# Kernel optimization log

Hardware: AMD Instinct MI355X
Metric: run time of the kernel (lower is better)

The kernel has to match this reference:

```python
import jax, jax.numpy as jnp
import numpy as np

D_MODEL = 1024
NUM_HEADS = 16
D_IN = 1024

def setup_inputs() -> dict:
    key = jax.random.key(0)
    ks = jax.random.split(key, 5)
    scale = 1.0 / np.sqrt(D_IN)
    return {
        "in_features": jax.random.normal(ks[0], (4, 2048, D_IN), dtype=jnp.float32),
        "q_weight": jax.random.normal(ks[1], (D_MODEL, D_IN), dtype=jnp.float32) * scale,
        "k_weight": jax.random.normal(ks[2], (D_MODEL, D_IN), dtype=jnp.float32) * scale,
        "v_weight": jax.random.normal(ks[3], (D_MODEL, D_IN), dtype=jnp.float32) * scale,
        "o_weight": jax.random.normal(ks[4], (D_MODEL, D_MODEL), dtype=jnp.float32) * scale,
    }

def reference(in_features, q_weight, k_weight, v_weight, o_weight):
    batch, seq_len, _ = in_features.shape
    d_head = D_MODEL // NUM_HEADS
    # QKV projections (Linear with no bias: x @ W^T)
    q = jnp.einsum('bsi,di->bsd', in_features, q_weight)
    k = jnp.einsum('bsi,di->bsd', in_features, k_weight)
    v = jnp.einsum('bsi,di->bsd', in_features, v_weight)
    # split heads -> [b, h, s, d_head]
    q = q.reshape(batch, seq_len, NUM_HEADS, d_head).transpose(0, 2, 1, 3)
    k = k.reshape(batch, seq_len, NUM_HEADS, d_head).transpose(0, 2, 1, 3)
    v = v.reshape(batch, seq_len, NUM_HEADS, d_head).transpose(0, 2, 1, 3)
    # scaled dot-product attention (scale by per-head dim, as in SelfAttention)
    scores = jnp.einsum('bhqd,bhkd->bhqk', q, k) / jnp.sqrt(jnp.float32(d_head))
    probs = jax.nn.softmax(scores, axis=-1)
    ctx = jnp.einsum('bhqk,bhkd->bhqd', probs, v)
    # merge heads -> [b, s, d_model]
    ctx = ctx.transpose(0, 2, 1, 3).reshape(batch, seq_len, D_MODEL)
    # output projection
    return jnp.einsum('bsd,md->bsm', ctx, o_weight)
```

## Files before the change

kernel.cpp:

```cpp
#include <hip/hip_runtime.h>

typedef _Float16 half8 __attribute__((ext_vector_type(8)));
typedef _Float16 half4v __attribute__((ext_vector_type(4)));
typedef float f32x4 __attribute__((ext_vector_type(4)));
typedef float f32x16 __attribute__((ext_vector_type(16)));

__device__ __forceinline__ void gload_lds16(const _Float16* g, _Float16* l) {
    __builtin_amdgcn_global_load_lds(
        (const __attribute__((address_space(1))) void*)g,
        (__attribute__((address_space(3))) void*)l,
        16, 0, 0);
}

__global__ void cvt_f32_f16(const float* __restrict__ src, _Float16* __restrict__ dst, int n4) {
    int i = blockIdx.x * blockDim.x + threadIdx.x;
    if (i >= n4) return;
    f32x4 v = ((const f32x4*)src)[i];
    half4v h;
    h[0] = (_Float16)v[0]; h[1] = (_Float16)v[1];
    h[2] = (_Float16)v[2]; h[3] = (_Float16)v[3];
    ((half4v*)dst)[i] = h;
}

template<int MODE>
__global__ void gemm_nt(const _Float16* __restrict__ A,
                        const _Float16* __restrict__ Wbase,
                        void* __restrict__ outbase)
{
    constexpr int K = 1024;
    __shared__ _Float16 As[2][128 * 32];
    __shared__ _Float16 Bs[2][128 * 32];

    const int tid  = threadIdx.x;
    const int lane = tid & 63;
    const int w    = tid >> 6;
    const int wr   = w >> 1, wc = w & 1;
    const int lr   = lane & 15, lg = lane >> 4;
    const int brow = blockIdx.x * 128;
    const int bcol = blockIdx.y * 128;

    const _Float16* Bw = Wbase + (MODE == 0 ? (size_t)blockIdx.z * (1024u * 1024u) : 0);

    const int srow = w * 16 + (lane >> 2);
    const int scol = (lane & 3) * 8;
    const _Float16* Ag = A  + (size_t)(brow + srow) * K + scol;
    const _Float16* Bg = Bw + (size_t)(bcol + srow) * K + scol;

    auto stage = [&](int buf, int kt) {
        const _Float16* a0 = Ag + kt * 32;
        const _Float16* b0 = Bg + kt * 32;
        gload_lds16(a0,           &As[buf][w * 512]);
        gload_lds16(a0 + 64 * K,  &As[buf][w * 512 + 2048]);
        gload_lds16(b0,           &Bs[buf][w * 512]);
        gload_lds16(b0 + 64 * K,  &Bs[buf][w * 512 + 2048]);
    };

    f32x4 acc[4][4] = {};
    stage(0, 0);
    __syncthreads();

    for (int kt = 0; kt < K / 32; ++kt) {
        const int cur = kt & 1;
        if (kt + 1 < K / 32) stage(cur ^ 1, kt + 1);
        half8 af[4], bf[4];
#pragma unroll
        for (int mi = 0; mi < 4; ++mi)
            af[mi] = *(const half8*)&As[cur][(wr * 64 + mi * 16 + lr) * 32 + lg * 8];
#pragma unroll
        for (int ni = 0; ni < 4; ++ni)
            bf[ni] = *(const half8*)&Bs[cur][(wc * 64 + ni * 16 + lr) * 32 + lg * 8];
#pragma unroll
        for (int mi = 0; mi < 4; ++mi)
#pragma unroll
            for (int ni = 0; ni < 4; ++ni)
                acc[mi][ni] = __builtin_amdgcn_mfma_f32_16x16x32_f16(af[mi], bf[ni], acc[mi][ni], 0, 0, 0);
        __syncthreads();
    }

    if (MODE == 0) {
        _Float16* outp = (_Float16*)outbase + (size_t)blockIdx.z * (8192u * 1024u);
        if (blockIdx.z == 2) {
            _Float16* Ts = &As[0][0];
#pragma unroll
            for (int p = 0; p < 2; ++p) {
                if (wc == p) {
#pragma unroll
                    for (int mi = 0; mi < 4; ++mi)
#pragma unroll
                        for (int ni = 0; ni < 4; ++ni) {
                            int drow = ni * 16 + lr;
                            int s0   = wr * 64 + mi * 16 + lg * 4;
                            half4v o;
#pragma unroll
                            for (int r = 0; r < 4; ++r) o[r] = (_Float16)acc[mi][ni][r];
                            int byteoff = drow * 256 + s0 * 2;
                            byteoff ^= (drow & 7) << 4;
                            *(half4v*)((char*)Ts + byteoff) = o;
                        }
                }
                __syncthreads();
                {
                    int row   = tid >> 2;
                    int cbase = (tid & 3) * 4;
                    int gd = bcol + p * 64 + row;
                    int h = gd >> 6, dd = gd & 63;
                    int b = brow >> 11, sseq = brow & 2047;
                    _Float16* gout = outp + (((size_t)b * 16 + h) * 64 + dd) * 2048 + sseq;
#pragma unroll
                    for (int j = 0; j < 4; ++j) {
                        int c  = cbase + j;
                        int lc = c ^ (row & 7);
                        half8 v = *(const half8*)&Ts[row * 128 + lc * 8];
                        *(half8*)&gout[c * 8] = v;
                    }
                }
                __syncthreads();
            }
        } else {
            const float scale = (blockIdx.z == 0) ? 0.18033688f : 1.0f;
#pragma unroll
            for (int mi = 0; mi < 4; ++mi)
#pragma unroll
                for (int ni = 0; ni < 4; ++ni)
#pragma unroll
                    for (int r = 0; r < 4; ++r) {
                        int row = brow + wr * 64 + mi * 16 + lg * 4 + r;
                        int col = bcol + wc * 64 + ni * 16 + lr;
                        int b = row >> 11, s = row & 2047;
                        int h = col >> 6,  d = col & 63;
                        outp[(((size_t)b * 16 + h) * 2048 + s) * 64 + d] =
                            (_Float16)(acc[mi][ni][r] * scale);
                    }
        }
    } else {
        float* outp = (float*)outbase;
#pragma unroll
        for (int mi = 0; mi < 4; ++mi)
#pragma unroll
            for (int ni = 0; ni < 4; ++ni)
#pragma unroll
                for (int r = 0; r < 4; ++r) {
                    int row = brow + wr * 64 + mi * 16 + lg * 4 + r;
                    int col = bcol + wc * 64 + ni * 16 + lr;
                    outp[(size_t)row * 1024 + col] = acc[mi][ni][r];
                }
    }
}

__global__ __launch_bounds__(256, 4)
void attn_kernel(const _Float16* __restrict__ Q,
                 const _Float16* __restrict__ Kx,
                 const _Float16* __restrict__ Vt,
                 _Float16* __restrict__ Ctx)
{
    __shared__ _Float16 Ks[2][64 * 72];
    __shared__ _Float16 Vs[2][64 * 72];

    const int tid = threadIdx.x, lane = tid & 63, w = tid >> 6;
    const int l31 = lane & 31, hi = lane >> 5;
    const int bh = blockIdx.y, qblk = blockIdx.x;

    const _Float16* Qp  = Q  + ((size_t)bh * 2048 + qblk * 128) * 64;
    const _Float16* Kp  = Kx + (size_t)bh * 2048 * 64;
    const _Float16* Vtp = Vt + (size_t)bh * 64 * 2048;

    half8 qf[4];
#pragma unroll
    for (int ks = 0; ks < 4; ++ks)
        qf[ks] = *(const half8*)(Qp + (size_t)(w * 32 + l31) * 64 + ks * 16 + hi * 8);

    const int srow = tid >> 3;
    const int scol = (tid & 7) * 8;
    const _Float16* Kg0 = Kp  + (size_t)srow * 64   + scol;
    const _Float16* Vg0 = Vtp + (size_t)srow * 2048 + scol;
    const int ldso = srow * 72 + scol;

    f32x16 cacc[2] = {};
    float m = -1e30f, l = 0.f;

    half8 kr0, kr1, vr0, vr1;
    kr0 = *(const half8*)(Kg0);
    kr1 = *(const half8*)(Kg0 + 32 * 64);
    vr0 = *(const half8*)(Vg0);
    vr1 = *(const half8*)(Vg0 + 32 * 2048);
    *(half8*)&Ks[0][ldso]           = kr0;
    *(half8*)&Ks[0][ldso + 32 * 72] = kr1;
    *(half8*)&Vs[0][ldso]           = vr0;
    *(half8*)&Vs[0][ldso + 32 * 72] = vr1;
    __syncthreads();

    for (int t = 0; t < 32; ++t) {
        const int cur = t & 1;
        if (t < 31) {
            kr0 = *(const half8*)(Kg0 + (size_t)(t + 1) * 4096);
            kr1 = *(const half8*)(Kg0 + (size_t)(t + 1) * 4096 + 32 * 64);
        }

        f32x16 sf[2];
        __builtin_amdgcn_s_setprio(1);
#pragma unroll
        for (int kt = 0; kt < 2; ++kt) {
            f32x16 z = {};
#pragma unroll
            for (int ks = 0; ks < 4; ++ks) {
                half8 kf = *(const half8*)&Ks[cur][(kt * 32 + l31) * 72 + ks * 16 + hi * 8];
                z = __builtin_amdgcn_mfma_f32_32x32x16_f16(kf, qf[ks], z, 0, 0, 0);
            }
            sf[kt] = z;
        }
        __builtin_amdgcn_s_setprio(0);

        if (t < 31) {
            *(half8*)&Ks[cur ^ 1][ldso]           = kr0;
            *(half8*)&Ks[cur ^ 1][ldso + 32 * 72] = kr1;
            vr0 = *(const half8*)(Vg0 + (t + 1) * 64);
            vr1 = *(const half8*)(Vg0 + (t + 1) * 64 + 32 * 2048);
        }

        float pmax = -1e30f;
#pragma unroll
        for (int kt = 0; kt < 2; ++kt)
#pragma unroll
            for (int r = 0; r < 16; ++r) pmax = fmaxf(pmax, sf[kt][r]);
        pmax = fmaxf(pmax, __shfl_xor(pmax, 32, 64));

        if (!__all(pmax <= m + 8.0f)) {
            float mn = fmaxf(m, pmax);
            float sc = __builtin_amdgcn_exp2f(m - mn);
            cacc[0] = cacc[0] * sc;
            cacc[1] = cacc[1] * sc;
            l *= sc;
            m = mn;
        }

        float rsum = 0.f;
#pragma unroll
        for (int kt = 0; kt < 2; ++kt)
#pragma unroll
            for (int r = 0; r < 16; ++r) {
                float p = __builtin_amdgcn_exp2f(sf[kt][r] - m);
                sf[kt][r] = p;
                rsum += p;
            }
        rsum += __shfl_xor(rsum, 32, 64);
        l += rsum;

        unsigned uq[2][4][2];
#pragma unroll
        for (int kt = 0; kt < 2; ++kt)
#pragma unroll
            for (int qd = 0; qd < 4; ++qd)
#pragma unroll
                for (int w2 = 0; w2 < 2; ++w2)
                    uq[kt][qd][w2] = __builtin_bit_cast(unsigned,
                        __builtin_amdgcn_cvt_pkrtz(sf[kt][4 * qd + 2 * w2],
                                                   sf[kt][4 * qd + 2 * w2 + 1]));

        half8 bf[4];
#pragma unroll
        for (int ks = 0; ks < 4; ++ks) {
            const int kt = ks >> 1, k1 = ks & 1;
            union { half8 h; unsigned u[4]; } bu;
#pragma unroll
            for (int w2 = 0; w2 < 2; ++w2) {
                unsigned a = uq[kt][2 * k1][w2];
                unsigned b = uq[kt][2 * k1 + 1][w2];
                unsigned send = hi ? a : b;
                unsigned recv = (unsigned)__shfl_xor((int)send, 32, 64);
                bu.u[w2]     = hi ? recv : a;
                bu.u[2 + w2] = hi ? b : recv;
            }
            bf[ks] = bu.h;
        }

        __builtin_amdgcn_s_setprio(1);
#pragma unroll
        for (int dt = 0; dt < 2; ++dt)
#pragma unroll
            for (int ks = 0; ks < 4; ++ks) {
                half8 vf = *(const half8*)&Vs[cur][(dt * 32 + l31) * 72 + ks * 16 + hi * 8];
                cacc[dt] = __builtin_amdgcn_mfma_f32_32x32x16_f16(vf, bf[ks], cacc[dt], 0, 0, 0);
            }
        __builtin_amdgcn_s_setprio(0);

        if (t < 31) {
            *(half8*)&Vs[cur ^ 1][ldso]           = vr0;
            *(half8*)&Vs[cur ^ 1][ldso + 32 * 72] = vr1;
        }
        __syncthreads();
    }

    const float inv = 1.0f / l;
    const int s = qblk * 128 + w * 32 + l31;
    _Float16* Cp = Ctx + ((size_t)(bh >> 4) * 2048 + s) * 1024 + (bh & 15) * 64;
#pragma unroll
    for (int dt = 0; dt < 2; ++dt)
#pragma unroll
        for (int qd = 0; qd < 4; ++qd) {
            half4v o;
#pragma unroll
            for (int j = 0; j < 4; ++j) o[j] = (_Float16)(cacc[dt][4 * qd + j] * inv);
            *(half4v*)&Cp[dt * 32 + qd * 8 + hi * 4] = o;
        }
}

extern "C" void kernel_launch(void* const* d_in, const int* in_sizes, int n_in,
                              void* d_out, int out_size, void* d_ws, size_t ws_size,
                              hipStream_t stream)
{
    const float* X  = (const float*)d_in[0];
    const float* Wq = (const float*)d_in[1];
    const float* Wk = (const float*)d_in[2];
    const float* Wv = (const float*)d_in[3];
    const float* Wo = (const float*)d_in[4];

    if (ws_size < (size_t)(8 + 4 + 24) * 1024 * 1024 * 2) return;
    _Float16* Xh  = (_Float16*)d_ws;
    _Float16* Wh  = Xh + (size_t)8 * 1024 * 1024;
    _Float16* QKV = Wh + (size_t)4 * 1024 * 1024;
    _Float16* Ctx = Xh;

    cvt_f32_f16<<<8192, 256, 0, stream>>>(X,  Xh,            2097152);
    cvt_f32_f16<<<1024, 256, 0, stream>>>(Wq, Wh,            262144);
    cvt_f32_f16<<<1024, 256, 0, stream>>>(Wk, Wh + 1048576,  262144);
    cvt_f32_f16<<<1024, 256, 0, stream>>>(Wv, Wh + 2097152,  262144);
    cvt_f32_f16<<<1024, 256, 0, stream>>>(Wo, Wh + 3145728,  262144);

    gemm_nt<0><<<dim3(64, 8, 3), 256, 0, stream>>>(Xh, Wh, QKV);

    attn_kernel<<<dim3(16, 64), 256, 0, stream>>>(QKV, QKV + 8388608, QKV + 16777216, Ctx);

    gemm_nt<1><<<dim3(64, 8, 1), 256, 0, stream>>>(Ctx, Wh + 3145728, d_out);
}
```

Baseline: 214.9 us.

## Compute softmax row sums via MFMA with ones and batch weight conversions

The attention kernel no longer accumulates the softmax denominator with scalar adds and a cross-lane shuffle. It instead runs four extra MFMAs that multiply a ones vector by the packed fp16 probabilities, which puts the row sum into an accumulator. The row-max reduction is also restructured as a tree to shorten the dependency chain. Separately, the four weight conversion launches are merged into one launch with a 2D grid, cutting launch overhead. The trade-off is extra MFMA work and 16 more accumulator registers, and the sum now comes from fp16-rounded probabilities.

```diff
diff --git a/kernel.cpp b/kernel.cpp
--- a/kernel.cpp
+++ b/kernel.cpp
@@ -20,6 +20,19 @@
     h[0] = (_Float16)v[0]; h[1] = (_Float16)v[1];
     h[2] = (_Float16)v[2]; h[3] = (_Float16)v[3];
     ((half4v*)dst)[i] = h;
+}
+
+__global__ void cvt4_f32_f16(const float* __restrict__ s0, const float* __restrict__ s1,
+                             const float* __restrict__ s2, const float* __restrict__ s3,
+                             _Float16* __restrict__ dst) {
+    int i = blockIdx.x * blockDim.x + threadIdx.x;
+    int wsel = blockIdx.y;
+    const float* src = (wsel == 0) ? s0 : (wsel == 1) ? s1 : (wsel == 2) ? s2 : s3;
+    f32x4 v = ((const f32x4*)src)[i];
+    half4v h;
+    h[0] = (_Float16)v[0]; h[1] = (_Float16)v[1];
+    h[2] = (_Float16)v[2]; h[3] = (_Float16)v[3];
+    ((half4v*)(dst + (size_t)wsel * 1048576))[i] = h;
 }
 
 template<int MODE>
@@ -169,6 +182,10 @@
     for (int ks = 0; ks < 4; ++ks)
         qf[ks] = *(const half8*)(Qp + (size_t)(w * 32 + l31) * 64 + ks * 16 + hi * 8);
 
+    half8 ones;
+#pragma unroll
+    for (int e = 0; e < 8; ++e) ones[e] = (_Float16)1.0f;
+
     const int srow = tid >> 3;
     const int scol = (tid & 7) * 8;
     const _Float16* Kg0 = Kp  + (size_t)srow * 64   + scol;
@@ -176,7 +193,8 @@
     const int ldso = srow * 72 + scol;
 
     f32x16 cacc[2] = {};
-    float m = -1e30f, l = 0.f;
+    f32x16 lsum = {};
+    float m = -1e30f;
 
     half8 kr0, kr1, vr0, vr1;
     kr0 = *(const half8*)(Kg0);
@@ -217,11 +235,13 @@
             vr1 = *(const half8*)(Vg0 + (t + 1) * 64 + 32 * 2048);
         }
 
-        float pmax = -1e30f;
-#pragma unroll
-        for (int kt = 0; kt < 2; ++kt)
-#pragma unroll
-            for (int r = 0; r < 16; ++r) pmax = fmaxf(pmax, sf[kt][r]);
+        float t8[8];
+#pragma unroll
+        for (int r = 0; r < 8; ++r)
+            t8[r] = fmaxf(fmaxf(sf[0][r], sf[0][r + 8]), fmaxf(sf[1][r], sf[1][r + 8]));
+#pragma unroll
+        for (int r = 0; r < 4; ++r) t8[r] = fmaxf(t8[r], t8[r + 4]);
+        float pmax = fmaxf(fmaxf(t8[0], t8[2]), fmaxf(t8[1], t8[3]));
         pmax = fmaxf(pmax, __shfl_xor(pmax, 32, 64));
 
         if (!__all(pmax <= m + 8.0f)) {
@@ -229,21 +249,15 @@
             float sc = __builtin_amdgcn_exp2f(m - mn);
             cacc[0] = cacc[0] * sc;
             cacc[1] = cacc[1] * sc;
-            l *= sc;
+            lsum = lsum * sc;
             m = mn;
         }
 
-        float rsum = 0.f;
 #pragma unroll
         for (int kt = 0; kt < 2; ++kt)
 #pragma unroll
-            for (int r = 0; r < 16; ++r) {
-                float p = __builtin_amdgcn_exp2f(sf[kt][r] - m);
-                sf[kt][r] = p;
-                rsum += p;
-            }
-        rsum += __shfl_xor(rsum, 32, 64);
-        l += rsum;
+            for (int r = 0; r < 16; ++r)
+                sf[kt][r] = __builtin_amdgcn_exp2f(sf[kt][r] - m);
 
         unsigned uq[2][4][2];
 #pragma unroll
@@ -281,6 +295,9 @@
                 half8 vf = *(const half8*)&Vs[cur][(dt * 32 + l31) * 72 + ks * 16 + hi * 8];
                 cacc[dt] = __builtin_amdgcn_mfma_f32_32x32x16_f16(vf, bf[ks], cacc[dt], 0, 0, 0);
             }
+#pragma unroll
+        for (int ks = 0; ks < 4; ++ks)
+            lsum = __builtin_amdgcn_mfma_f32_32x32x16_f16(ones, bf[ks], lsum, 0, 0, 0);
         __builtin_amdgcn_s_setprio(0);
 
         if (t < 31) {
@@ -290,7 +307,7 @@
         __syncthreads();
     }
 
-    const float inv = 1.0f / l;
+    const float inv = 1.0f / lsum[0];
     const int s = qblk * 128 + w * 32 + l31;
     _Float16* Cp = Ctx + ((size_t)(bh >> 4) * 2048 + s) * 1024 + (bh & 15) * 64;
 #pragma unroll
@@ -320,11 +337,8 @@
     _Float16* QKV = Wh + (size_t)4 * 1024 * 1024;
     _Float16* Ctx = Xh;
 
-    cvt_f32_f16<<<8192, 256, 0, stream>>>(X,  Xh,            2097152);
-    cvt_f32_f16<<<1024, 256, 0, stream>>>(Wq, Wh,            262144);
-    cvt_f32_f16<<<1024, 256, 0, stream>>>(Wk, Wh + 1048576,  262144);
-    cvt_f32_f16<<<1024, 256, 0, stream>>>(Wv, Wh + 2097152,  262144);
-    cvt_f32_f16<<<1024, 256, 0, stream>>>(Wo, Wh + 3145728,  262144);
+    cvt_f32_f16<<<8192, 256, 0, stream>>>(X, Xh, 2097152);
+    cvt4_f32_f16<<<dim3(1024, 4), 256, 0, stream>>>(Wq, Wk, Wv, Wo, Wh);
 
     gemm_nt<0><<<dim3(64, 8, 3), 256, 0, stream>>>(Xh, Wh, QKV);
 
```

After: 220.5 us. +2.6%, slower.
